# Kernel optimization log

Measured on AMD Instinct MI355X. Metric: run time of the kernel, lower is better.

Reference implementation:

```python
import jax, jax.numpy as jnp
import numpy as np
import math

NUM_HEADS = 16
KEY_SIZE = 64
HIDDEN = 4096
EMBED = 1024
VOCAB = 32000
SEQ = 2048
LAYERS = 4


def rmsnorm(x):
    return x * jax.lax.rsqrt(jnp.mean(x * x, axis=-1, keepdims=True) + 1e-5)


def rope_buffers(seq, d):
    half = d // 2
    i = jnp.arange(d)
    offset = i % half
    scales = jnp.power(10000.0, (-2.0 / d) * offset.astype(jnp.float32))
    m = jnp.arange(seq, dtype=jnp.float32)
    angles = m[:, None] * scales[None, :]  # [S, D]
    cos = jnp.cos(angles)
    sin = jnp.sin(angles)
    sin = jnp.concatenate([-sin[:, :half], sin[:, half:]], axis=-1)
    return cos, sin


def rotate(x, cos, sin):
    # x: [B, H, S, D]; cos/sin: [S, D]
    half = KEY_SIZE // 2
    swapped = jnp.concatenate([x[..., half:], x[..., :half]], axis=-1)
    return cos[None, None] * x + sin[None, None] * swapped


def setup_inputs() -> dict:
    key = jax.random.key(0)
    ks = jax.random.split(key, 7)
    std = 0.02
    return {
        'tokens': jax.random.randint(ks[0], (1, SEQ), 0, VOCAB),
        'table': jax.random.normal(ks[1], (VOCAB, EMBED), jnp.float32) * std,
        'qkv_w': jax.random.normal(ks[2], (LAYERS, EMBED, 3 * NUM_HEADS * KEY_SIZE), jnp.float32) * std,
        'out_w': jax.random.normal(ks[3], (LAYERS, NUM_HEADS * KEY_SIZE, EMBED), jnp.float32) * std,
        'up_w': jax.random.normal(ks[4], (LAYERS, EMBED, 2 * HIDDEN), jnp.float32) * std,
        'down_w': jax.random.normal(ks[5], (LAYERS, HIDDEN, EMBED), jnp.float32) * std,
        'vocab_w': jax.random.normal(ks[6], (EMBED, VOCAB), jnp.float32) * std,
    }


def reference(tokens, table, qkv_w, out_w, up_w, down_w, vocab_w):
    B, S = tokens.shape
    H, D = NUM_HEADS, KEY_SIZE
    # module zeroes embedding row 0 each forward
    table = table.at[0].set(0.0)
    cos, sin = rope_buffers(S, D)
    causal = jnp.tril(jnp.ones((S, S), dtype=bool))  # context_size == S -> pure causal
    emb = table[tokens]  # [B, S, E]
    for l in range(LAYERS):
        # --- self attention ---
        normed = rmsnorm(emb)
        qkv = normed @ qkv_w[l]  # [B, S, 3HD]
        q, k, v = jnp.split(qkv, 3, axis=-1)
        q = q.reshape(B, S, H, D).transpose(0, 2, 1, 3)
        k = k.reshape(B, S, H, D).transpose(0, 2, 1, 3)
        v = v.reshape(B, S, H, D).transpose(0, 2, 1, 3)
        q = rotate(q, cos, sin)
        k = rotate(k, cos, sin)
        attn = jnp.einsum('bhqd,bhkd->bhqk', q, k) / math.sqrt(D)
        attn = jnp.where(causal[None, None], attn, -jnp.inf)
        attn = jax.nn.softmax(attn, axis=-1)
        out = jnp.einsum('bhqk,bhkd->bhqd', attn, v)
        out = out.transpose(0, 2, 1, 3).reshape(B, S, H * D)
        emb = emb + out @ out_w[l]
        # --- SwiGLU FFN ---
        normed = rmsnorm(emb)
        gate_up = normed @ up_w[l]
        gate, up = gate_up[..., :HIDDEN], gate_up[..., HIDDEN:]
        emb = emb + (up * jax.nn.silu(gate)) @ down_w[l]
    emb = rmsnorm(emb)
    logits = emb @ vocab_w  # [B, S, V]
    return logits
```

## Files before the change

### kernel.cpp

```cpp
#include <hip/hip_runtime.h>
#include <hip/hip_bf16.h>

typedef __attribute__((ext_vector_type(8))) short short8;
typedef __attribute__((ext_vector_type(4))) float f32x4;

__device__ __forceinline__ ushort f2bf(float f) {
  uint32_t u = __float_as_uint(f);
  uint32_t r = (u + 0x7FFFu + ((u >> 16) & 1u)) >> 16;
  return (ushort)r;
}
__device__ __forceinline__ float bf2f(ushort u) {
  return __uint_as_float(((uint32_t)u) << 16);
}

__device__ __forceinline__ void gload_lds16(const ushort* g, ushort* l) {
  __builtin_amdgcn_global_load_lds(
      (const __attribute__((address_space(1))) void*)g,
      (__attribute__((address_space(3))) void*)l, 16, 0, 0);
}

__device__ __forceinline__ f32x4 mfma16(short8 a, short8 b, f32x4 c) {
  return __builtin_amdgcn_mfma_f32_16x16x32_bf16(a, b, c, 0, 0, 0);
}

#define BAR() __builtin_amdgcn_s_barrier()
#define WAIT_LGKM()                                        \
  do {                                                     \
    asm volatile("s_waitcnt lgkmcnt(0)" ::: "memory");     \
    __builtin_amdgcn_sched_barrier(0);                     \
  } while (0)
#define WAIT_VM0()                                         \
  do {                                                     \
    asm volatile("s_waitcnt vmcnt(0)" ::: "memory");       \
    __builtin_amdgcn_sched_barrier(0);                     \
  } while (0)
#define WAIT_VM4()                                         \
  do {                                                     \
    asm volatile("s_waitcnt vmcnt(4)" ::: "memory");       \
    __builtin_amdgcn_sched_barrier(0);                     \
  } while (0)

__global__ __launch_bounds__(256)
void transpose_conv_kernel(const float* __restrict__ W, ushort* __restrict__ WT,
                           const int K, const int N, const int mode) {
  const size_t lofs = (size_t)blockIdx.z * K * N;
  W += lofs;
  WT += lofs;
  __shared__ float tile[64][65];
  const int n0 = blockIdx.x * 64;
  const int k0 = blockIdx.y * 64;
  const int t = threadIdx.x;
#pragma unroll
  for (int j = 0; j < 4; ++j) {
    const int idx = j * 1024 + t * 4;
    const int kk = idx >> 6, nn = idx & 63;
    *(float4*)&tile[kk][nn] = *(const float4*)&W[(size_t)(k0 + kk) * N + n0 + nn];
  }
  __syncthreads();
#pragma unroll
  for (int j = 0; j < 4; ++j) {
    const int idx = j * 1024 + t * 4;
    const int nn = idx >> 6, kk = idx & 63;
    int rr = n0 + nn;
    if (mode == 1) rr = (rr < 4096) ? (2 * rr) : (2 * (rr - 4096) + 1);
    ushort4 o;
    o.x = f2bf(tile[kk + 0][nn]);
    o.y = f2bf(tile[kk + 1][nn]);
    o.z = f2bf(tile[kk + 2][nn]);
    o.w = f2bf(tile[kk + 3][nn]);
    *(ushort4*)&WT[(size_t)rr * K + k0 + kk] = o;
  }
}

__global__ __launch_bounds__(256)
void sincos_kernel(float2* __restrict__ cstab) {
  const int idx = blockIdx.x * 256 + threadIdx.x;
  const int s = idx >> 5, o = idx & 31;
  const float freq = exp2f(-0.41524101186092029f * (float)o);
  const float a = (float)s * freq;
  cstab[idx] = make_float2(cosf(a), sinf(a));
}

__global__ __launch_bounds__(256)
void embed_norm_kernel(const int* __restrict__ tokens, const float* __restrict__ table,
                       float* __restrict__ emb, ushort* __restrict__ normed) {
  const int s = blockIdx.x, t = threadIdx.x;
  const int tok = tokens[s];
  float4 v = make_float4(0.f, 0.f, 0.f, 0.f);
  if (tok != 0) v = *(const float4*)&table[(size_t)tok * 1024 + t * 4];
  *(float4*)&emb[(size_t)s * 1024 + t * 4] = v;
  float ss = v.x * v.x + v.y * v.y + v.z * v.z + v.w * v.w;
#pragma unroll
  for (int off = 32; off; off >>= 1) ss += __shfl_xor(ss, off);
  __shared__ float red[4];
  if ((t & 63) == 0) red[t >> 6] = ss;
  __syncthreads();
  const float total = red[0] + red[1] + red[2] + red[3];
  const float sc = rsqrtf(total * (1.f / 1024.f) + 1e-5f);
  ushort4 o;
  o.x = f2bf(v.x * sc); o.y = f2bf(v.y * sc);
  o.z = f2bf(v.z * sc); o.w = f2bf(v.w * sc);
  *(ushort4*)&normed[(size_t)s * 1024 + t * 4] = o;
}

__global__ __launch_bounds__(256)
void rmsnorm_kernel(const float* __restrict__ x, ushort* __restrict__ out) {
  const int row = blockIdx.x, t = threadIdx.x;
  const float4 v = *(const float4*)&x[(size_t)row * 1024 + t * 4];
  float ss = v.x * v.x + v.y * v.y + v.z * v.z + v.w * v.w;
#pragma unroll
  for (int off = 32; off; off >>= 1) ss += __shfl_xor(ss, off);
  __shared__ float red[4];
  if ((t & 63) == 0) red[t >> 6] = ss;
  __syncthreads();
  const float total = red[0] + red[1] + red[2] + red[3];
  const float sc = rsqrtf(total * (1.f / 1024.f) + 1e-5f);
  ushort4 o;
  o.x = f2bf(v.x * sc); o.y = f2bf(v.y * sc);
  o.z = f2bf(v.z * sc); o.w = f2bf(v.w * sc);
  *(ushort4*)&out[(size_t)row * 1024 + t * 4] = o;
}

__global__ __launch_bounds__(512)
void attn_mfma_kernel(const ushort* __restrict__ qh, const ushort* __restrict__ kh,
                      const ushort* __restrict__ vt, ushort* __restrict__ attn_out) {
  __shared__ ushort sQ[128 * 64];
  __shared__ ushort sK[64 * 64];
  __shared__ ushort sV[64 * 64];
  __shared__ ushort sP[8][1024];
  const int h = blockIdx.y;
  const int bx = blockIdx.x;
  const int qt = (h < 8) ? bx : 15 - bx;
  const int i0 = qt * 128;
  const int tid = threadIdx.x;
  const int w = tid >> 6, lane = tid & 63;
  const int llo = lane & 15, lhi = lane >> 4;
  const ushort* qg = qh + ((size_t)h * 2048 + i0) * 64;
  const ushort* kg = kh + (size_t)h * 2048 * 64;
  const ushort* vg = vt + (size_t)h * 64 * 2048;

#pragma unroll
  for (int j = 0; j < 2; ++j) {
    const int cb = j * 512 + w * 64;
    const int ch = cb + lane;
    const int row = ch >> 3, c = ch & 7;
    gload_lds16(qg + (size_t)row * 64 + ((c ^ (row & 7)) * 8), &sQ[cb * 8]);
  }
  __syncthreads();
  const int qrow = w * 16 + llo;
  const short8 qf0 = *(const short8*)&sQ[qrow * 64 + ((lhi ^ (qrow & 7)) * 8)];
  const short8 qf1 = *(const short8*)&sQ[qrow * 64 + (((4 + lhi) ^ (qrow & 7)) * 8)];
  const int wmax = i0 + w * 16 + 15;

  float m = -1e30f, lsum = 0.f;
  f32x4 o[4] = {};
  const int nch = 2 * qt + 2;
  for (int cb2 = 0; cb2 < nch; ++cb2) {
    const int kb = cb2 * 64;
    __syncthreads();
    {
      const int cb = w * 64;
      const int ch = cb + lane;
      const int row = ch >> 3, c = ch & 7;
      gload_lds16(kg + (size_t)(kb + row) * 64 + ((c ^ (row & 7)) * 8), &sK[cb * 8]);
      gload_lds16(vg + (size_t)row * 2048 + kb + ((c ^ (row & 7)) * 8), &sV[cb * 8]);
    }
    __syncthreads();

    if (kb > wmax) continue;

    f32x4 st[4] = {};
#pragma unroll
    for (int ck = 0; ck < 2; ++ck) {
      const short8 qf = ck ? qf1 : qf0;
#pragma unroll
      for (int f = 0; f < 4; ++f) {
        const int key = f * 16 + llo;
        const short8 kf = *(const short8*)&sK[key * 64 + (((ck * 4 + lhi) ^ (key & 7)) * 8)];
        st[f] = mfma16(kf, qf, st[f]);
      }
    }

    float pv[4][4];
    const bool edge = (kb + 63 > i0 + w * 16);
#pragma unroll
    for (int f = 0; f < 4; ++f)
#pragma unroll
      for (int r = 0; r < 4; ++r) {
        float x = st[f][r] * 0.125f;
        if (edge && (kb - i0 + f * 16 + lhi * 4 + r) > qrow) x = -1e30f;
        pv[f][r] = x;
      }
    float mr = pv[0][0];
#pragma unroll
    for (int f = 0; f < 4; ++f)
#pragma unroll
      for (int r = 0; r < 4; ++r) mr = fmaxf(mr, pv[f][r]);
    mr = fmaxf(mr, __shfl_xor(mr, 16));
    mr = fmaxf(mr, __shfl_xor(mr, 32));
    const float mnew = fmaxf(m, mr);
    const float scale = __expf(m - mnew);
    m = mnew;
    float rs = 0.f;
#pragma unroll
    for (int f = 0; f < 4; ++f)
#pragma unroll
      for (int r = 0; r < 4; ++r) {
        const float p = __expf(pv[f][r] - mnew);
        pv[f][r] = p;
        rs += p;
      }
    rs += __shfl_xor(rs, 16);
    rs += __shfl_xor(rs, 32);
    lsum = lsum * scale + rs;
    float scr[4];
#pragma unroll
    for (int r = 0; r < 4; ++r) scr[r] = __shfl(scale, lhi * 4 + r);
#pragma unroll
    for (int nn = 0; nn < 4; ++nn)
#pragma unroll
      for (int r = 0; r < 4; ++r) o[nn][r] *= scr[r];

    ushort* pw = sP[w];
#pragma unroll
    for (int f = 0; f < 4; ++f) {
      uint2 pk;
      pk.x = (uint)f2bf(pv[f][0]) | ((uint)f2bf(pv[f][1]) << 16);
      pk.y = (uint)f2bf(pv[f][2]) | ((uint)f2bf(pv[f][3]) << 16);
      *(uint2*)&pw[llo * 64 + ((f * 16 + lhi * 4) ^ ((llo & 7) << 3))] = pk;
    }
    const short8 pf0 = *(const short8*)&pw[llo * 64 + ((lhi ^ (llo & 7)) * 8)];
    const short8 pf1 = *(const short8*)&pw[llo * 64 + (((4 + lhi) ^ (llo & 7)) * 8)];

#pragma unroll
    for (int ck = 0; ck < 2; ++ck) {
      const short8 pf = ck ? pf1 : pf0;
#pragma unroll
      for (int nn = 0; nn < 4; ++nn) {
        const int drow = nn * 16 + llo;
        const short8 vf = *(const short8*)&sV[drow * 64 + (((ck * 4 + lhi) ^ (drow & 7)) * 8)];
        o[nn] = mfma16(pf, vf, o[nn]);
      }
    }
  }

  const float inv = 1.f / lsum;
  float invr[4];
#pragma unroll
  for (int r = 0; r < 4; ++r) invr[r] = __shfl(inv, lhi * 4 + r);
#pragma unroll
  for (int nn = 0; nn < 4; ++nn)
#pragma unroll
    for (int r = 0; r < 4; ++r) {
      const int row = i0 + w * 16 + lhi * 4 + r;
      attn_out[(size_t)row * 1024 + h * 64 + nn * 16 + llo] = f2bf(o[nn][r] * invr[r]);
    }
}

template <int BM, int BN, int EPI>
__global__ __launch_bounds__(256)
void gemm_bt64_kernel(const ushort* __restrict__ A, const ushort* __restrict__ BT,
                      const float* __restrict__ addend, void* __restrict__ Cout,
                      const int M, const int N, const int K) {
  constexpr int WM = BM / 2, WN = BN / 2;
  constexpr int FM = WM / 16, FN = WN / 16;
  __shared__ ushort sA[BM * 64];
  __shared__ ushort sB[BN * 64];
  const int bm0 = blockIdx.y * BM;
  const int bn0 = blockIdx.x * BN;
  const int tid = threadIdx.x;
  const int wid = tid >> 6, lane = tid & 63;
  const int wr = wid >> 1, wc = wid & 1;
  const int lhi = lane >> 4, llo = lane & 15;
  f32x4 acc[FM][FN] = {};
  for (int kt = 0; kt < K; kt += 64) {
#pragma unroll
    for (int i = 0; i < BM * 8 / 256; ++i) {
      const int cb = i * 256 + wid * 64;
      const int ch = cb + lane;
      const int row = ch >> 3, c = ch & 7;
      gload_lds16(A + (size_t)(bm0 + row) * K + kt + ((c ^ (row & 7)) * 8),
                  sA + (size_t)cb * 8);
    }
#pragma unroll
    for (int i = 0; i < BN * 8 / 256; ++i) {
      const int cb = i * 256 + wid * 64;
      const int ch = cb + lane;
      const int row = ch >> 3, c = ch & 7;
      gload_lds16(BT + (size_t)(bn0 + row) * K + kt + ((c ^ (row & 7)) * 8),
                  sB + (size_t)cb * 8);
    }
    __syncthreads();
    short8 aF[FM][2], bF[FN][2];
#pragma unroll
    for (int mm = 0; mm < FM; ++mm) {
      const int row = wr * WM + mm * 16 + llo;
#pragma unroll
      for (int ks = 0; ks < 2; ++ks)
        aF[mm][ks] = *(const short8*)&sA[row * 64 + (((ks * 4 + lhi) ^ (row & 7)) * 8)];
    }
#pragma unroll
    for (int nn = 0; nn < FN; ++nn) {
      const int row = wc * WN + nn * 16 + llo;
#pragma unroll
      for (int ks = 0; ks < 2; ++ks)
        bF[nn][ks] = *(const short8*)&sB[row * 64 + (((ks * 4 + lhi) ^ (row & 7)) * 8)];
    }
#pragma unroll
    for (int mm = 0; mm < FM; ++mm)
#pragma unroll
      for (int nn = 0; nn < FN; ++nn)
#pragma unroll
        for (int ks = 0; ks < 2; ++ks)
          acc[mm][nn] = mfma16(aF[mm][ks], bF[nn][ks], acc[mm][nn]);
    __syncthreads();
  }
#pragma unroll
  for (int mm = 0; mm < FM; ++mm) {
#pragma unroll
    for (int nn = 0; nn < FN; ++nn) {
      const int col = bn0 + wc * WN + nn * 16 + llo;
#pragma unroll
      for (int r = 0; r < 4; ++r) {
        const int row = bm0 + wr * WM + mm * 16 + lhi * 4 + r;
        float v = acc[mm][nn][r];
        if constexpr (EPI == 1) v += addend[(size_t)row * N + col];
        ((float*)Cout)[(size_t)row * N + col] = v;
      }
    }
  }
}

__global__ __launch_bounds__(256)
void gemm_qkv_kernel(const ushort* __restrict__ A, const ushort* __restrict__ BT,
                     const float2* __restrict__ cstab, ushort* __restrict__ qh,
                     ushort* __restrict__ kh, ushort* __restrict__ vt, const int K) {
  constexpr int BM = 128, BN = 128, WM = 64, WN = 64, FM = 4, FN = 4;
  __shared__ ushort sA[BM * 64];
  __shared__ ushort sB[BN * 64];
  const int bm0 = blockIdx.y * BM;
  const int bn0 = blockIdx.x * BN;
  const int tid = threadIdx.x;
  const int wid = tid >> 6, lane = tid & 63;
  const int wr = wid >> 1, wc = wid & 1;
  const int lhi = lane >> 4, llo = lane & 15;
  f32x4 acc[FM][FN] = {};
  for (int kt = 0; kt < K; kt += 64) {
#pragma unroll
    for (int i = 0; i < 4; ++i) {
      const int cb = i * 256 + wid * 64;
      const int ch = cb + lane;
      const int row = ch >> 3, c = ch & 7;
      gload_lds16(A + (size_t)(bm0 + row) * K + kt + ((c ^ (row & 7)) * 8),
                  sA + (size_t)cb * 8);
    }
#pragma unroll
    for (int i = 0; i < 4; ++i) {
      const int cb = i * 256 + wid * 64;
      const int ch = cb + lane;
      const int row = ch >> 3, c = ch & 7;
      gload_lds16(BT + (size_t)(bn0 + row) * K + kt + ((c ^ (row & 7)) * 8),
                  sB + (size_t)cb * 8);
    }
    __syncthreads();
    short8 aF[FM][2], bF[FN][2];
#pragma unroll
    for (int mm = 0; mm < FM; ++mm) {
      const int row = wr * WM + mm * 16 + llo;
#pragma unroll
      for (int ks = 0; ks < 2; ++ks)
        aF[mm][ks] = *(const short8*)&sA[row * 64 + (((ks * 4 + lhi) ^ (row & 7)) * 8)];
    }
#pragma unroll
    for (int nn = 0; nn < FN; ++nn) {
      const int row = wc * WN + nn * 16 + llo;
#pragma unroll
      for (int ks = 0; ks < 2; ++ks)
        bF[nn][ks] = *(const short8*)&sB[row * 64 + (((ks * 4 + lhi) ^ (row & 7)) * 8)];
    }
#pragma unroll
    for (int mm = 0; mm < FM; ++mm)
#pragma unroll
      for (int nn = 0; nn < FN; ++nn)
#pragma unroll
        for (int ks = 0; ks < 2; ++ks)
          acc[mm][nn] = mfma16(aF[mm][ks], bF[nn][ks], acc[mm][nn]);
    __syncthreads();
  }
#pragma unroll
  for (int mm = 0; mm < FM; ++mm) {
    const int row_base = bm0 + wr * WM + mm * 16 + lhi * 4;
#pragma unroll
    for (int nn = 0; nn < FN; ++nn) {
      const int col = bn0 + wc * WN + nn * 16 + llo;
      const int part = col >> 10;
      const int hcol = col & 1023;
      const int h = hcol >> 6;
      const int d = hcol & 63;
      const int off = d & 31;
      if (part == 2) {
        ushort4 o;
        o.x = f2bf(acc[mm][nn][0]);
        o.y = f2bf(acc[mm][nn][1]);
        o.z = f2bf(acc[mm][nn][2]);
        o.w = f2bf(acc[mm][nn][3]);
        *(ushort4*)&vt[((size_t)h * 64 + d) * 2048 + row_base] = o;
      } else {
#pragma unroll
        for (int r = 0; r < 4; ++r) {
          const int row = row_base + r;
          const float v = acc[mm][nn][r];
          const float pt = acc[mm][nn ^ 2][r];
          const float2 cn = cstab[row * 32 + off];
          const float si = (d < 32) ? -cn.y : cn.y;
          const ushort o = f2bf(cn.x * v + si * pt);
          const size_t ho = ((size_t)h * 2048 + row) * 64 + d;
          if (part == 0) qh[ho] = o; else kh[ho] = o;
        }
      }
    }
  }
}

#define LDA_(MH)                                                              \
  {                                                                           \
    _Pragma("unroll") for (int mm = 0; mm < 4; ++mm) {                        \
      const int row = wr * 128 + ((MH) * 4 + mm) * 16 + llo;                  \
      _Pragma("unroll") for (int ks = 0; ks < 2; ++ks)                        \
          aF[mm][ks] = *(const short8*)&cA[row * 64 +                         \
                          (((ks * 4 + lhi) ^ (row & 7)) * 8)];                \
    }                                                                         \
  }
#define LDB_(NH)                                                              \
  {                                                                           \
    _Pragma("unroll") for (int nn = 0; nn < 2; ++nn) {                        \
      const int row = wc * 64 + ((NH) * 2 + nn) * 16 + llo;                   \
      _Pragma("unroll") for (int ks = 0; ks < 2; ++ks)                        \
          bF[nn][ks] = *(const short8*)&cB[row * 64 +                         \
                          (((ks * 4 + lhi) ^ (row & 7)) * 8)];                \
    }                                                                         \
  }
#define MFMAQ_(MH, NH)                                                        \
  {                                                                           \
    __builtin_amdgcn_s_setprio(1);                                            \
    _Pragma("unroll") for (int mm = 0; mm < 4; ++mm)                          \
        _Pragma("unroll") for (int nn = 0; nn < 2; ++nn)                      \
            _Pragma("unroll") for (int ks = 0; ks < 2; ++ks)                  \
                acc[(MH) * 4 + mm][(NH) * 2 + nn] =                           \
                    mfma16(aF[mm][ks], bF[nn][ks],                            \
                           acc[(MH) * 4 + mm][(NH) * 2 + nn]);                \
    __builtin_amdgcn_s_setprio(0);                                            \
  }

template <int EPI>
__global__ __launch_bounds__(512, 2)
void gemm8_kernel(const ushort* __restrict__ A, const ushort* __restrict__ BT,
                  void* __restrict__ Cout,
                  const int M, const int N, const int K, const int nby) {
  extern __shared__ ushort smem[];
  const int nwg = gridDim.x;
  const int cpx = nwg >> 3;
  int id = blockIdx.x;
  id = (id & 7) * cpx + (id >> 3);
  const int by = id % nby, bx = id / nby;
  const int bm0 = by * 256, bn0 = bx * 256;
  const int tid = threadIdx.x;
  const int wid = tid >> 6, lane = tid & 63;
  const int wr = wid >> 2, wc = wid & 3;
  const int llo = lane & 15, lhi = lane >> 4;
  const ushort* gA = A + (size_t)bm0 * K;
  const ushort* gB = BT + (size_t)bn0 * K;

  auto stage = [&](const ushort* g, ushort* dst, int kt) {
#pragma unroll
    for (int i = 0; i < 4; ++i) {
      const int chunk = i * 512 + wid * 64 + lane;
      const int row = chunk >> 3, c = chunk & 7;
      gload_lds16(g + (size_t)row * K + kt + ((c ^ (row & 7)) * 8),
                  dst + (size_t)(i * 512 + wid * 64) * 8);
    }
  };

  f32x4 acc[8][4] = {};
  short8 aF[4][2];
  short8 bF[2][2];

  stage(gA, smem, 0);
  stage(gB, smem + 16384, 0);
  WAIT_VM0();
  BAR();

  const int nt = K >> 6;
  for (int t = 0; t < nt; ++t) {
    const int cur = t & 1;
    ushort* cA = smem + cur * 32768;
    ushort* cB = cA + 16384;
    ushort* nA = smem + (cur ^ 1) * 32768;
    ushort* nB = nA + 16384;
    const bool pf = (t + 1 < nt);
    LDA_(0); LDB_(0);
    if (pf) { stage(gA, nA, (t + 1) * 64); stage(gB, nB, (t + 1) * 64); }
    BAR(); WAIT_LGKM();
    MFMAQ_(0, 0);
    BAR();
    LDB_(1);
    BAR(); WAIT_LGKM();
    MFMAQ_(0, 1);
    BAR();
    LDA_(1);
    BAR(); WAIT_LGKM();
    MFMAQ_(1, 1);
    BAR();
    LDB_(0);
    BAR(); WAIT_LGKM();
    MFMAQ_(1, 0);
    if (pf) WAIT_VM0();
    BAR();
  }

#pragma unroll
  for (int m = 0; m < 8; ++m) {
#pragma unroll
    for (int n = 0; n < 4; ++n) {
      const int col = bn0 + wc * 64 + n * 16 + llo;
#pragma unroll
      for (int r = 0; r < 4; ++r) {
        const int row = bm0 + wr * 128 + m * 16 + lhi * 4 + r;
        float v = acc[m][n][r];
        if constexpr (EPI == 3) {
          const float other = __shfl_xor(v, 1);
          if ((llo & 1) == 0) {
            const float gate = v, up = other;
            const float hh = up * gate / (1.f + expf(-gate));
            ((ushort*)Cout)[(size_t)row * (N >> 1) + (col >> 1)] = f2bf(hh);
          }
        } else {
          ((float*)Cout)[(size_t)row * N + col] = v;
        }
      }
    }
  }
}

template <int EPI>
__global__ __launch_bounds__(512, 2)
void gemm8p_kernel(const ushort* __restrict__ A, const ushort* __restrict__ BT,
                   void* __restrict__ Cout,
                   const int M, const int N, const int K, const int nby) {
  extern __shared__ ushort smem[];
  const int nwg = gridDim.x;
  const int cpx = nwg >> 3;
  int id = blockIdx.x;
  id = (id & 7) * cpx + (id >> 3);
  const int by = id % nby, bx = id / nby;
  const int bm0 = by * 256, bn0 = bx * 256;
  const int tid = threadIdx.x;
  const int wid = tid >> 6, lane = tid & 63;
  const int wr = wid >> 2, wc = wid & 3;
  const int llo = lane & 15, lhi = lane >> 4;
  const ushort* gA = A + (size_t)bm0 * K;
  const ushort* gB = BT + (size_t)bn0 * K;

  auto stage = [&](ushort* dst, int kt) {
#pragma unroll
    for (int i = 0; i < 2; ++i) {
      const int cb = i * 512 + wid * 64;
      const int ch = cb + lane;
      const int row = ch >> 2, c = ch & 3;
      gload_lds16(gA + (size_t)row * K + kt + ((c ^ ((row >> 1) & 3)) * 8),
                  dst + (size_t)cb * 8);
    }
#pragma unroll
    for (int i = 0; i < 2; ++i) {
      const int cb = i * 512 + wid * 64;
      const int ch = cb + lane;
      const int row = ch >> 2, c = ch & 3;
      gload_lds16(gB + (size_t)row * K + kt + ((c ^ ((row >> 1) & 3)) * 8),
                  dst + 8192 + (size_t)cb * 8);
    }
  };

  f32x4 acc[8][4] = {};
  short8 aF[4], bF[4];

  const int nt = K >> 5;
  stage(smem, 0);
  stage(smem + 16384, 32);
  WAIT_VM4();
  BAR();

  int cs = 0;
  for (int t = 0; t < nt; ++t) {
    ushort* cA = smem + cs * 16384;
    ushort* cB = cA + 8192;
    int ss = cs + 2; if (ss >= 3) ss -= 3;
    const bool pf2 = (t + 2 < nt);
    if (pf2) stage(smem + ss * 16384, (t + 2) * 32);
#pragma unroll
    for (int mm = 0; mm < 4; ++mm) {
      const int row = wr * 128 + mm * 16 + llo;
      aF[mm] = *(const short8*)&cA[row * 32 + ((lhi ^ ((row >> 1) & 3)) * 8)];
    }
#pragma unroll
    for (int nn = 0; nn < 4; ++nn) {
      const int row = wc * 64 + nn * 16 + llo;
      bF[nn] = *(const short8*)&cB[row * 32 + ((lhi ^ ((row >> 1) & 3)) * 8)];
    }
    BAR(); WAIT_LGKM();
    __builtin_amdgcn_s_setprio(1);
#pragma unroll
    for (int mm = 0; mm < 4; ++mm)
#pragma unroll
      for (int nn = 0; nn < 4; ++nn)
        acc[mm][nn] = mfma16(aF[mm], bF[nn], acc[mm][nn]);
    __builtin_amdgcn_s_setprio(0);
    BAR();
#pragma unroll
    for (int mm = 0; mm < 4; ++mm) {
      const int row = wr * 128 + (mm + 4) * 16 + llo;
      aF[mm] = *(const short8*)&cA[row * 32 + ((lhi ^ ((row >> 1) & 3)) * 8)];
    }
    BAR(); WAIT_LGKM();
    __builtin_amdgcn_s_setprio(1);
#pragma unroll
    for (int mm = 0; mm < 4; ++mm)
#pragma unroll
      for (int nn = 0; nn < 4; ++nn)
        acc[mm + 4][nn] = mfma16(aF[mm], bF[nn], acc[mm + 4][nn]);
    __builtin_amdgcn_s_setprio(0);
    if (pf2) { WAIT_VM4(); } else { WAIT_VM0(); }
    BAR();
    ++cs; if (cs == 3) cs = 0;
  }

#pragma unroll
  for (int m = 0; m < 8; ++m) {
#pragma unroll
    for (int n = 0; n < 4; ++n) {
      const int col = bn0 + wc * 64 + n * 16 + llo;
#pragma unroll
      for (int r = 0; r < 4; ++r) {
        const int row = bm0 + wr * 128 + m * 16 + lhi * 4 + r;
        ((float*)Cout)[(size_t)row * N + col] = acc[m][n][r];
      }
    }
  }
}

extern "C" void kernel_launch(void* const* d_in, const int* in_sizes, int n_in,
                              void* d_out, int out_size, void* d_ws, size_t ws_size,
                              hipStream_t stream) {
  const int* tokens    = (const int*)d_in[0];
  const float* table   = (const float*)d_in[1];
  const float* qkv_w   = (const float*)d_in[2];
  const float* out_w   = (const float*)d_in[3];
  const float* up_w    = (const float*)d_in[4];
  const float* down_w  = (const float*)d_in[5];
  const float* vocab_w = (const float*)d_in[6];
  float* logits = (float*)d_out;

  constexpr int G8_LDS = 131072;
  constexpr int G8P_LDS = 98304;
  hipFuncSetAttribute(reinterpret_cast<const void*>(&gemm8_kernel<3>),
                      hipFuncAttributeMaxDynamicSharedMemorySize, G8_LDS);
  hipFuncSetAttribute(reinterpret_cast<const void*>(&gemm8p_kernel<0>),
                      hipFuncAttributeMaxDynamicSharedMemorySize, G8P_LDS);

  char* p = (char*)d_ws;
  auto alloc = [&](size_t bytes) {
    char* r = p;
    p += (bytes + 255) & ~(size_t)255;
    return r;
  };
  float*  emb    = (float*)alloc(2048ull * 1024 * 4);
  ushort* normed = (ushort*)alloc(2048ull * 1024 * 2);
  float2* cstab  = (float2*)alloc(2048ull * 32 * 8);
  ushort* qhb    = (ushort*)alloc(16ull * 2048 * 64 * 2);
  ushort* khb    = (ushort*)alloc(16ull * 2048 * 64 * 2);
  ushort* vtb    = (ushort*)alloc(16ull * 64 * 2048 * 2);
  ushort* attno  = (ushort*)alloc(2048ull * 1024 * 2);
  ushort* hbuf   = (ushort*)alloc(2048ull * 4096 * 2);
  ushort* qkvT   = (ushort*)alloc(4ull * 3072 * 1024 * 2);
  ushort* outT   = (ushort*)alloc(4ull * 1024 * 1024 * 2);
  ushort* upT    = (ushort*)alloc(4ull * 8192 * 1024 * 2);
  ushort* downT  = (ushort*)alloc(4ull * 1024 * 4096 * 2);
  ushort* vocabT = (ushort*)alloc(32000ull * 1024 * 2);

  transpose_conv_kernel<<<dim3(3072 / 64, 1024 / 64, 4), 256, 0, stream>>>(
      qkv_w, qkvT, 1024, 3072, 0);
  transpose_conv_kernel<<<dim3(1024 / 64, 1024 / 64, 4), 256, 0, stream>>>(
      out_w, outT, 1024, 1024, 0);
  transpose_conv_kernel<<<dim3(8192 / 64, 1024 / 64, 4), 256, 0, stream>>>(
      up_w, upT, 1024, 8192, 1);
  transpose_conv_kernel<<<dim3(1024 / 64, 4096 / 64, 4), 256, 0, stream>>>(
      down_w, downT, 4096, 1024, 0);
  transpose_conv_kernel<<<dim3(32000 / 64, 1024 / 64, 1), 256, 0, stream>>>(
      vocab_w, vocabT, 1024, 32000, 0);
  sincos_kernel<<<256, 256, 0, stream>>>(cstab);

  embed_norm_kernel<<<2048, 256, 0, stream>>>(tokens, table, emb, normed);

  for (int l = 0; l < 4; ++l) {
    if (l > 0) rmsnorm_kernel<<<2048, 256, 0, stream>>>(emb, normed);
    gemm_qkv_kernel<<<dim3(3072 / 128, 2048 / 128), 256, 0, stream>>>(
        normed, qkvT + (size_t)l * 3072 * 1024, cstab, qhb, khb, vtb, 1024);
    attn_mfma_kernel<<<dim3(16, 16), 512, 0, stream>>>(qhb, khb, vtb, attno);
    gemm_bt64_kernel<64, 128, 1><<<dim3(1024 / 128, 2048 / 64), 256, 0, stream>>>(
        attno, outT + (size_t)l * 1024 * 1024, emb, emb, 2048, 1024, 1024);
    rmsnorm_kernel<<<2048, 256, 0, stream>>>(emb, normed);
    gemm8_kernel<3><<<(8192 / 256) * (2048 / 256), 512, G8_LDS, stream>>>(
        normed, upT + (size_t)l * 8192 * 1024, hbuf, 2048, 8192, 1024, 2048 / 256);
    gemm_bt64_kernel<64, 128, 1><<<dim3(1024 / 128, 2048 / 64), 256, 0, stream>>>(
        hbuf, downT + (size_t)l * 1024 * 4096, emb, emb, 2048, 1024, 4096);
  }
  rmsnorm_kernel<<<2048, 256, 0, stream>>>(emb, normed);
  gemm8p_kernel<0><<<(32000 / 256) * (2048 / 256), 512, G8P_LDS, stream>>>(
      normed, vocabT, logits, 2048, 32000, 1024, 2048 / 256);
}
```

Baseline: 1.293 ms.

## Split attention KV range across two blocks and merge partial softmax results

Each attention block's key range is split into two halves processed by separate blocks, doubling the grid from 256 to 512 blocks to improve occupancy across compute units. Partial unnormalized outputs and running max/sum are written to fp32 workspace, and a new merge kernel combines them with log-sum-exp rescaling into bf16 output. This adds an extra kernel launch and fp32 workspace traffic in exchange for better parallelism.

```diff
diff --git a/kernel.cpp b/kernel.cpp
--- a/kernel.cpp
+++ b/kernel.cpp
@@ -123,14 +123,16 @@
 
 __global__ __launch_bounds__(512)
 void attn_mfma_kernel(const ushort* __restrict__ qh, const ushort* __restrict__ kh,
-                      const ushort* __restrict__ vt, ushort* __restrict__ attn_out) {
+                      const ushort* __restrict__ vt, float* __restrict__ wso,
+                      float* __restrict__ wsml) {
   __shared__ ushort sQ[128 * 64];
   __shared__ ushort sK[64 * 64];
   __shared__ ushort sV[64 * 64];
   __shared__ ushort sP[8][1024];
   const int h = blockIdx.y;
-  const int bx = blockIdx.x;
-  const int qt = (h < 8) ? bx : 15 - bx;
+  const int u = blockIdx.x;
+  const int qt_raw = u >> 1, half = u & 1;
+  const int qt = (h < 8) ? qt_raw : 15 - qt_raw;
   const int i0 = qt * 128;
   const int tid = threadIdx.x;
   const int w = tid >> 6, lane = tid & 63;
@@ -154,8 +156,9 @@
 
   float m = -1e30f, lsum = 0.f;
   f32x4 o[4] = {};
-  const int nch = 2 * qt + 2;
-  for (int cb2 = 0; cb2 < nch; ++cb2) {
+  const int c0 = half ? (qt + 1) : 0;
+  const int c1 = half ? (2 * qt + 2) : (qt + 1);
+  for (int cb2 = c0; cb2 < c1; ++cb2) {
     const int kb = cb2 * 64;
     __syncthreads();
     {
@@ -244,17 +247,38 @@
     }
   }
 
-  const float inv = 1.f / lsum;
-  float invr[4];
-#pragma unroll
-  for (int r = 0; r < 4; ++r) invr[r] = __shfl(inv, lhi * 4 + r);
 #pragma unroll
   for (int nn = 0; nn < 4; ++nn)
 #pragma unroll
     for (int r = 0; r < 4; ++r) {
       const int row = i0 + w * 16 + lhi * 4 + r;
-      attn_out[(size_t)row * 1024 + h * 64 + nn * 16 + llo] = f2bf(o[nn][r] * invr[r]);
-    }
+      wso[((size_t)(half * 16 + h) * 2048 + row) * 64 + nn * 16 + llo] = o[nn][r];
+    }
+  if (lhi == 0) {
+    const int row = i0 + w * 16 + llo;
+    *(float2*)&wsml[((size_t)(half * 16 + h) * 2048 + row) * 2] = make_float2(m, lsum);
+  }
+}
+
+__global__ __launch_bounds__(256)
+void attn_merge_kernel(const float* __restrict__ wso, const float* __restrict__ wsml,
+                       ushort* __restrict__ attn_out) {
+  const int row = blockIdx.x;
+  const int t = threadIdx.x;
+  const int h = t >> 4, dg = t & 15;
+  const float2 ml1 = *(const float2*)&wsml[((size_t)h * 2048 + row) * 2];
+  const float2 ml2 = *(const float2*)&wsml[((size_t)(16 + h) * 2048 + row) * 2];
+  const float m = fmaxf(ml1.x, ml2.x);
+  const float w1 = __expf(ml1.x - m), w2 = __expf(ml2.x - m);
+  const float inv = 1.f / (ml1.y * w1 + ml2.y * w2);
+  const float4 o1 = *(const float4*)&wso[((size_t)h * 2048 + row) * 64 + dg * 4];
+  const float4 o2 = *(const float4*)&wso[((size_t)(16 + h) * 2048 + row) * 64 + dg * 4];
+  ushort4 o;
+  o.x = f2bf((o1.x * w1 + o2.x * w2) * inv);
+  o.y = f2bf((o1.y * w1 + o2.y * w2) * inv);
+  o.z = f2bf((o1.z * w1 + o2.z * w2) * inv);
+  o.w = f2bf((o1.w * w1 + o2.w * w2) * inv);
+  *(ushort4*)&attn_out[(size_t)row * 1024 + h * 64 + dg * 4] = o;
 }
 
 template <int BM, int BN, int EPI>
@@ -679,6 +703,8 @@
   ushort* khb    = (ushort*)alloc(16ull * 2048 * 64 * 2);
   ushort* vtb    = (ushort*)alloc(16ull * 64 * 2048 * 2);
   ushort* attno  = (ushort*)alloc(2048ull * 1024 * 2);
+  float*  wso    = (float*)alloc(2ull * 16 * 2048 * 64 * 4);
+  float*  wsml   = (float*)alloc(2ull * 16 * 2048 * 2 * 4);
   ushort* hbuf   = (ushort*)alloc(2048ull * 4096 * 2);
   ushort* qkvT   = (ushort*)alloc(4ull * 3072 * 1024 * 2);
   ushort* outT   = (ushort*)alloc(4ull * 1024 * 1024 * 2);
@@ -704,7 +730,8 @@
     if (l > 0) rmsnorm_kernel<<<2048, 256, 0, stream>>>(emb, normed);
     gemm_qkv_kernel<<<dim3(3072 / 128, 2048 / 128), 256, 0, stream>>>(
         normed, qkvT + (size_t)l * 3072 * 1024, cstab, qhb, khb, vtb, 1024);
-    attn_mfma_kernel<<<dim3(16, 16), 512, 0, stream>>>(qhb, khb, vtb, attno);
+    attn_mfma_kernel<<<dim3(32, 16), 512, 0, stream>>>(qhb, khb, vtb, wso, wsml);
+    attn_merge_kernel<<<2048, 256, 0, stream>>>(wso, wsml, attno);
     gemm_bt64_kernel<64, 128, 1><<<dim3(1024 / 128, 2048 / 64), 256, 0, stream>>>(
         attno, outT + (size_t)l * 1024 * 1024, emb, emb, 2048, 1024, 1024);
     rmsnorm_kernel<<<2048, 256, 0, stream>>>(emb, normed);
```

After: 1.205 ms. 1.07x faster.
